# Kernel optimization log

Hardware: AMD Instinct MI355X
Metric: run time of the kernel (lower is better)

Reference implementation:

```python
import jax, jax.numpy as jnp
import numpy as np

C_IN, C_OUT = 64, 32
SD, RFF = 2, 16
RF = 0.05          # receptive_field percentile
TEMP = 1.0
EPS = 1e-8
RFF_STD = 6.0


def setup_inputs() -> dict:
    key = jax.random.key(0)
    ks = jax.random.split(key, 10)
    B_, T, V, Q = 2, 4, 2048, 512
    x = jax.random.normal(ks[0], (B_, T, V, C_IN), dtype=jnp.float32)
    pos = jax.random.uniform(ks[1], (V, SD), dtype=jnp.float32)
    query_pos = jax.random.uniform(ks[2], (Q, SD), dtype=jnp.float32)
    s = 1.0 / np.sqrt(C_IN)
    W_lin = jax.random.uniform(ks[3], (C_IN, C_IN), minval=-s, maxval=s, dtype=jnp.float32)
    b_lin = jax.random.uniform(ks[4], (C_IN,), minval=-s, maxval=s, dtype=jnp.float32)
    Bmat = RFF_STD * jax.random.normal(ks[5], (SD, RFF), dtype=jnp.float32)
    s1 = 1.0 / np.sqrt(32)
    W1 = jax.random.uniform(ks[6], (32, 32), minval=-s1, maxval=s1, dtype=jnp.float32)
    b1 = jax.random.uniform(ks[7], (32,), minval=-s1, maxval=s1, dtype=jnp.float32)
    W2 = jax.random.uniform(ks[8], (C_IN * C_OUT, 32), minval=-s1, maxval=s1, dtype=jnp.float32)
    sf = np.sqrt(3.0 / C_IN)
    filt = jax.random.uniform(ks[9], (C_IN * C_OUT,), minval=-sf, maxval=sf, dtype=jnp.float32)
    bias = jnp.zeros((C_OUT,), dtype=jnp.float32)
    return {"x": x, "pos": pos, "query_pos": query_pos, "W_lin": W_lin, "b_lin": b_lin,
            "Bmat": Bmat, "W1": W1, "b1": b1, "W2": W2, "filt": filt, "bias": bias}


def reference(x, pos, query_pos, W_lin, b_lin, Bmat, W1, b1, W2, filt, bias):
    # pairwise periodic displacement / squared distance
    dist = query_pos[:, None, :] - pos[None, :, :]            # (Q, V, 2)
    dist = (dist + 0.5) % 1.0 - 0.5                           # periodic wrap
    edist = jnp.sum(dist ** 2, axis=-1)                       # (Q, V)
    # quantile threshold -> max neighbourhood size (eager, data-dependent like torch)
    thr = jnp.quantile(edist, RF, axis=-1, keepdims=True)     # linear interpolation, as torch
    K = int(jnp.max(jnp.sum(edist <= thr, axis=-1)))
    _, ind = jax.lax.top_k(-edist, K)                         # (Q, K) nearest neighbours
    # gather per-query neighbour displacements / distances
    d_g = jnp.take_along_axis(dist, ind[..., None], axis=1)   # (Q, K, 2)
    e_g = jnp.take_along_axis(edist, ind, axis=1)[..., None]  # (Q, K, 1)
    e_g = e_g - jnp.min(e_g, axis=-2, keepdims=True)
    e_g = e_g / (jnp.max(e_g, axis=-2, keepdims=True) + EPS)
    k_dist = jax.nn.softmax(-e_g / TEMP, axis=-2)             # (Q, K, 1)
    # random Fourier features + kernel MLP
    proj = 2.0 * jnp.pi * (d_g @ Bmat)                        # (Q, K, 16)
    kfeat = jnp.concatenate([jnp.sin(proj), jnp.cos(proj)], axis=-1)  # (Q, K, 32)
    h = jax.nn.gelu(kfeat @ W1.T + b1, approximate=False)
    ker = (h @ W2.T + filt) * k_dist                          # (Q, K, C_IN*C_OUT)
    ker = ker.reshape(ker.shape[0], ker.shape[1], C_IN, C_OUT)
    # point-wise linear on features, then gather + contract
    xl = x @ W_lin.T + b_lin                                  # (B, T, V, C_IN)
    xg = xl[:, :, ind, :]                                     # (B, T, Q, K, C_IN)
    return jnp.einsum('qvcd,btqvc->btqd', ker, xg) + bias     # (B, T, Q, C_OUT)
```

## Files before the change

### kernel.cpp

```cpp
#include <hip/hip_runtime.h>

#define K_SEL 103
typedef unsigned long long ull_t;
typedef _Float16 f16x8 __attribute__((ext_vector_type(8)));
typedef float f32x4 __attribute__((ext_vector_type(4)));

__global__ __launch_bounds__(256, 4) void k12(const float* __restrict__ pos,
                                              const float* __restrict__ qpos,
                                              const float* __restrict__ Bmat,
                                              const float* __restrict__ W1,
                                              const float* __restrict__ b1,
                                              _Float16* __restrict__ Hh,
                                              int* __restrict__ indg,
                                              float* __restrict__ invtot,
                                              const float* __restrict__ x,
                                              const float* __restrict__ W,
                                              const float* __restrict__ b,
                                              _Float16* __restrict__ xlh,
                                              const float* __restrict__ W2,
                                              const float* __restrict__ filt,
                                              _Float16* __restrict__ W2th) {
    __shared__ __align__(16) unsigned char smem[30848];
    const int tid = threadIdx.x;
    const int bid = blockIdx.x;
    const int lane = tid & 63;
    const int wid = tid >> 6;

    if (bid >= 512) {
        const int bb = bid - 512;
        float* Wt = (float*)smem;
        if (tid < 132) {
            int t = bb * 132 + tid;
            int d = t & 31;
            int e = t >> 5;
            int c = e & 63;
            int j = e >> 6;
            float v = (j < 32) ? W2[(c * 32 + d) * 32 + j] : filt[c * 32 + d];
            W2th[d * 2112 + e] = (_Float16)v;
        }
        for (int t = tid; t < 4096; t += 256)
            Wt[(t & 63) * 65 + (t >> 6)] = W[t];
        __syncthreads();
        const int i = tid & 63;
        const int sub = tid >> 6;
        const float bi = b[i];
        #pragma unroll
        for (int rr = 0; rr < 2; ++rr) {
            const int r0 = bb * 32 + rr * 16 + sub * 4;
            float acc0 = bi, acc1 = bi, acc2 = bi, acc3 = bi;
            const float* xr = x + (size_t)r0 * 64;
            #pragma unroll 4
            for (int jj = 0; jj < 16; ++jj) {
                float4 v0 = *(const float4*)(xr + 0 * 64 + jj * 4);
                float4 v1 = *(const float4*)(xr + 1 * 64 + jj * 4);
                float4 v2 = *(const float4*)(xr + 2 * 64 + jj * 4);
                float4 v3 = *(const float4*)(xr + 3 * 64 + jj * 4);
                float w0 = Wt[(jj * 4 + 0) * 65 + i];
                float w1 = Wt[(jj * 4 + 1) * 65 + i];
                float w2 = Wt[(jj * 4 + 2) * 65 + i];
                float w3 = Wt[(jj * 4 + 3) * 65 + i];
                acc0 += v0.x * w0 + v0.y * w1 + v0.z * w2 + v0.w * w3;
                acc1 += v1.x * w0 + v1.y * w1 + v1.z * w2 + v1.w * w3;
                acc2 += v2.x * w0 + v2.y * w1 + v2.z * w2 + v2.w * w3;
                acc3 += v3.x * w0 + v3.y * w1 + v3.z * w2 + v3.w * w3;
            }
            xlh[(size_t)(r0 + 0) * 64 + i] = (_Float16)acc0;
            xlh[(size_t)(r0 + 1) * 64 + i] = (_Float16)acc1;
            xlh[(size_t)(r0 + 2) * 64 + i] = (_Float16)acc2;
            xlh[(size_t)(r0 + 3) * 64 + i] = (_Float16)acc3;
        }
        return;
    }

    const int q = bid;
    unsigned* ebits   = (unsigned*)(smem);
    unsigned* hist    = (unsigned*)(smem + 8192);
    _Float16* Hs      = (_Float16*)(smem + 8192);
    float*    W1s     = (float*)(smem + 24576);
    float*    b1s     = (float*)(smem + 28672);
    float*    Bm      = (float*)(smem + 28800);
    int*      sel_v   = (int*)(smem + 28928);
    float*    sel_e   = (float*)(smem + 29344);
    ull_t*    bnd     = (ull_t*)(smem + 29760);
    int*      counters= (int*)(smem + 30784);
    int*      info    = (int*)(smem + 30792);
    float*    wred    = (float*)(smem + 30800);
    float*    emax_s  = (float*)(smem + 30816);
    unsigned* wscan   = (unsigned*)(smem + 30824);

    for (int t = tid; t < 1024; t += 256) W1s[t] = W1[t];
    if (tid < 32) { b1s[tid] = b1[tid]; Bm[tid] = Bmat[tid]; }
    if (tid < 2)  counters[tid] = 0;
    for (int t = tid; t < 1024; t += 256) ((uint4*)hist)[t] = make_uint4(0, 0, 0, 0);
    const float qp0 = qpos[q * 2 + 0];
    const float qp1 = qpos[q * 2 + 1];
    __syncthreads();

    float lmin = 1e30f;
    for (int v = tid; v < 2048; v += 256) {
        float2 p = ((const float2*)pos)[v];
        float d0 = qp0 - p.x;
        float d1 = qp1 - p.y;
        d0 += 0.5f; d0 -= floorf(d0); d0 -= 0.5f;
        d1 += 0.5f; d1 -= floorf(d1); d1 -= 0.5f;
        float e = d0 * d0 + d1 * d1;
        ebits[v] = __float_as_uint(e);
        lmin = fminf(lmin, e);
        int bb2 = (int)(e * 8192.0f); bb2 = (bb2 > 4095) ? 4095 : bb2;
        atomicAdd(&hist[bb2], 1u);
    }
    #pragma unroll
    for (int off = 32; off > 0; off >>= 1)
        lmin = fminf(lmin, __shfl_xor(lmin, off, 64));
    if (lane == 0) wred[wid] = lmin;
    __syncthreads();
    const float e_min = fminf(fminf(wred[0], wred[1]), fminf(wred[2], wred[3]));

    unsigned lsum = 0;
    #pragma unroll
    for (int i = 0; i < 16; ++i) lsum += hist[tid * 16 + i];
    unsigned vq = lsum;
    #pragma unroll
    for (int off = 1; off < 64; off <<= 1) {
        unsigned n = __shfl_up(vq, off, 64);
        if (lane >= off) vq += n;
    }
    if (lane == 63) wscan[wid] = vq;
    __syncthreads();
    unsigned base = 0;
    for (int w2 = 0; w2 < wid; ++w2) base += wscan[w2];
    unsigned cum = base + vq - lsum;
    #pragma unroll
    for (int i = 0; i < 16; ++i) {
        unsigned cnt = hist[tid * 16 + i];
        if (cum <= 102u && 102u < cum + cnt) { info[0] = tid * 16 + i; info[1] = (int)cum; }
        cum += cnt;
    }
    __syncthreads();
    const int Bstar = info[0];
    const int L = info[1];
    const int need = K_SEL - L;

    {
        f16x8 z = {0, 0, 0, 0, 0, 0, 0, 0};
        for (int t = tid; t < 768; t += 256) ((f16x8*)Hs)[t] = z;
    }
    for (int v = tid; v < 2048; v += 256) {
        unsigned bb2 = ebits[v];
        float e = __uint_as_float(bb2);
        int bin = (int)(e * 8192.0f); bin = (bin > 4095) ? 4095 : bin;
        if (bin < Bstar) {
            int s2 = atomicAdd(&counters[0], 1);
            sel_v[s2] = v; sel_e[s2] = e;
        } else if (bin == Bstar) {
            int s2 = atomicAdd(&counters[1], 1);
            if (s2 < 128) bnd[s2] = (((ull_t)bb2) << 32) | (unsigned)v;
        }
    }
    __syncthreads();
    if (tid == 0) {
        int nb = counters[1]; if (nb > 128) nb = 128;
        for (int i = 1; i < nb; ++i) {
            ull_t key = bnd[i]; int j2 = i - 1;
            while (j2 >= 0 && bnd[j2] > key) { bnd[j2 + 1] = bnd[j2]; --j2; }
            bnd[j2 + 1] = key;
        }
        for (int i = 0; i < need; ++i) {
            sel_v[L + i] = (int)(unsigned)(bnd[i] & 0xffffffffull);
            sel_e[L + i] = __uint_as_float((unsigned)(bnd[i] >> 32));
        }
        emax_s[0] = __uint_as_float((unsigned)(bnd[need - 1] >> 32));
    }
    __syncthreads();

    const float denom = (emax_s[0] - e_min) + 1e-8f;
    float w = 0.0f;
    if (tid < K_SEL) {
        w = __expf(-(sel_e[tid] - e_min) / denom);
        sel_e[tid] = w;
    }
    float sw = w;
    #pragma unroll
    for (int off = 32; off > 0; off >>= 1)
        sw += __shfl_xor(sw, off, 64);
    if (lane == 0) wred[wid] = sw;
    __syncthreads();
    if (tid == 0)
        invtot[q] = 1.0f / (wred[0] + wred[1] + wred[2] + wred[3]);

    if (tid < 2 * K_SEL) {
        const int k = tid >> 1;
        const int io = (tid & 1) * 16;
        const int v = sel_v[k];
        const float wk = sel_e[k];
        float2 p = ((const float2*)pos)[v];
        float d0 = qp0 - p.x;
        float d1 = qp1 - p.y;
        d0 += 0.5f; d0 -= floorf(d0); d0 -= 0.5f;
        d1 += 0.5f; d1 -= floorf(d1); d1 -= 0.5f;
        float kf[32];
        #pragma unroll
        for (int f = 0; f < 16; ++f) {
            float t = d0 * Bm[f] + d1 * Bm[16 + f];
            float r = t - rintf(t);
            kf[f]      = __builtin_amdgcn_sinf(r);
            kf[16 + f] = __builtin_amdgcn_cosf(r);
        }
        #pragma unroll 4
        for (int i = io; i < io + 16; ++i) {
            float pre = b1s[i];
            #pragma unroll
            for (int jf = 0; jf < 32; ++jf) pre += kf[jf] * W1s[i * 32 + jf];
            float g = 0.5f * pre * (1.0f + erff(pre * 0.70710678118654752f));
            Hs[i * 128 + k] = (_Float16)(g * wk);
        }
        if (io == 0) {
            Hs[32 * 128 + k] = (_Float16)wk;
            indg[q * K_SEL + k] = v;
        }
    }
    __syncthreads();
    {
        _Float16* hq = Hh + (size_t)q * 6144;
        for (int t = tid; t < 768; t += 256)
            ((f16x8*)hq)[t] = ((const f16x8*)Hs)[t];
    }
}

__global__ __launch_bounds__(256, 4) void k3_main(const _Float16* __restrict__ xlh,
                                                  const _Float16* __restrict__ Hh,
                                                  const int* __restrict__ indg,
                                                  const _Float16* __restrict__ W2th,
                                                  const float* __restrict__ bias,
                                                  const float* __restrict__ invtot,
                                                  float* __restrict__ out) {
    const int bid = blockIdx.x;
    const int q = bid >> 1;
    const int bt0 = (bid & 1) * 4;
    const int tid = threadIdx.x;
    const int lane = tid & 63;
    const int wv = tid >> 6;
    const int n0 = lane & 15;
    const int quad = lane >> 4;

    __shared__ __align__(16) unsigned char smem[34944];
    _Float16* Xg  = (_Float16*)smem;
    _Float16* Zh4 = (_Float16*)(smem + 17536);
    int* ind_s    = (int*)(smem + 34432);
    float* red    = (float*)smem;

    const _Float16* hq = Hh + (size_t)q * 6144;
    f16x8 afr[4][3];
    #pragma unroll
    for (int ks = 0; ks < 4; ++ks)
        #pragma unroll
        for (int r = 0; r < 3; ++r)
            afr[ks][r] = *(const f16x8*)(hq + (r * 16 + n0) * 128 + ks * 32 + quad * 8);
    const float it = invtot[q];
    const int e0f = wv * 32 + quad * 8;
    f16x8 pf0 = *(const f16x8*)(W2th + (size_t)(0 * 16 + n0) * 2112 + e0f);
    f16x8 pf1 = *(const f16x8*)(W2th + (size_t)(1 * 16 + n0) * 2112 + e0f);
    if (tid < 128) {
        int kk = (tid < K_SEL) ? tid : tid - K_SEL;
        ind_s[tid] = indg[q * K_SEL + kk];
    }
    __syncthreads();

    int g_k[4], g_oct[4];
    #pragma unroll
    for (int i = 0; i < 4; ++i) {
        int t = tid + i * 256;
        g_k[i] = t >> 3;
        g_oct[i] = t & 7;
    }

    {
        f16x8 v0[4];
        #pragma unroll
        for (int i = 0; i < 4; ++i)
            v0[i] = *(const f16x8*)(xlh + ((size_t)bt0 * 2048 + ind_s[g_k[i]]) * 64 + g_oct[i] * 8);
        #pragma unroll
        for (int i = 0; i < 4; ++i) {
            int base = g_oct[i] * 1096 + g_k[i];
            #pragma unroll
            for (int jj = 0; jj < 8; ++jj) Xg[base + 136 * jj] = v0[i][jj];
        }
    }
    __syncthreads();

    const int cA = wv * 16 + n0;
    const int cswz = cA * 136 + ((cA >> 3) << 3);

    #pragma unroll
    for (int p = 0; p < 4; ++p) {
        f16x8 vn[4];
        if (p < 3) {
            #pragma unroll
            for (int i = 0; i < 4; ++i)
                vn[i] = *(const f16x8*)(xlh + ((size_t)(bt0 + p + 1) * 2048 + ind_s[g_k[i]]) * 64 + g_oct[i] * 8);
        }
        f32x4 Dz[3];
        #pragma unroll
        for (int r = 0; r < 3; ++r) Dz[r] = (f32x4){0.f, 0.f, 0.f, 0.f};
        #pragma unroll
        for (int ks = 0; ks < 4; ++ks) {
            f16x8 bfr = *(const f16x8*)(&Xg[cswz + ks * 32 + quad * 8]);
            #pragma unroll
            for (int r = 0; r < 3; ++r)
                Dz[r] = __builtin_amdgcn_mfma_f32_16x16x32_f16(afr[ks][r], bfr, Dz[r], 0, 0, 0);
        }
        __syncthreads();
        #pragma unroll
        for (int r = 0; r < 3; ++r)
            #pragma unroll
            for (int reg = 0; reg < 4; ++reg) {
                int j = r * 16 + quad * 4 + reg;
                if (j < 33) Zh4[p * 2112 + j * 64 + cA] = (_Float16)Dz[r][reg];
            }
        if (p < 3) {
            #pragma unroll
            for (int i = 0; i < 4; ++i) {
                int base = g_oct[i] * 1096 + g_k[i];
                #pragma unroll
                for (int jj = 0; jj < 8; ++jj) Xg[base + 136 * jj] = vn[i][jj];
            }
            __syncthreads();
        }
    }
    __syncthreads();

    f32x4 D2[2][2];
    #pragma unroll
    for (int pp = 0; pp < 2; ++pp)
        #pragma unroll
        for (int dt = 0; dt < 2; ++dt) D2[pp][dt] = (f32x4){0.f, 0.f, 0.f, 0.f};
    {
        f16x8 a2 = {0, 0, 0, 0, 0, 0, 0, 0};
        if (n0 < 4) a2 = *(const f16x8*)(&Zh4[n0 * 2112 + e0f]);
        D2[0][0] = __builtin_amdgcn_mfma_f32_16x16x32_f16(a2, pf0, D2[0][0], 0, 0, 0);
        D2[0][1] = __builtin_amdgcn_mfma_f32_16x16x32_f16(a2, pf1, D2[0][1], 0, 0, 0);
    }
    int pp = 1;
    #pragma unroll 2
    for (int s = wv + 4; s < 66; s += 4) {
        const int e0 = s * 32 + quad * 8;
        f16x8 a2 = {0, 0, 0, 0, 0, 0, 0, 0};
        if (n0 < 4) a2 = *(const f16x8*)(&Zh4[n0 * 2112 + e0]);
        #pragma unroll
        for (int dt = 0; dt < 2; ++dt) {
            f16x8 bfr = *(const f16x8*)(W2th + (size_t)(dt * 16 + n0) * 2112 + e0);
            D2[pp][dt] = __builtin_amdgcn_mfma_f32_16x16x32_f16(a2, bfr, D2[pp][dt], 0, 0, 0);
        }
        pp ^= 1;
    }
    #pragma unroll
    for (int dt = 0; dt < 2; ++dt)
        D2[0][dt] = D2[0][dt] + D2[1][dt];

    if (quad == 0) {
        #pragma unroll
        for (int dt = 0; dt < 2; ++dt)
            #pragma unroll
            for (int reg = 0; reg < 4; ++reg)
                red[((wv * 2 + dt) * 4 + reg) * 16 + n0] = D2[0][dt][reg];
    }
    __syncthreads();
    if (tid < 128) {
        const int bt = tid >> 5;
        const int d = tid & 31;
        const int dt = d >> 4;
        const int dn = d & 15;
        float s = 0.0f;
        #pragma unroll
        for (int w2 = 0; w2 < 4; ++w2)
            s += red[((w2 * 2 + dt) * 4 + bt) * 16 + dn];
        out[((size_t)(bt0 + bt) * 512 + q) * 32 + d] = bias[d] + it * s;
    }
}

extern "C" void kernel_launch(void* const* d_in, const int* in_sizes, int n_in,
                              void* d_out, int out_size, void* d_ws, size_t ws_size,
                              hipStream_t stream) {
    const float* x     = (const float*)d_in[0];
    const float* pos   = (const float*)d_in[1];
    const float* qpos  = (const float*)d_in[2];
    const float* W_lin = (const float*)d_in[3];
    const float* b_lin = (const float*)d_in[4];
    const float* Bmat  = (const float*)d_in[5];
    const float* W1    = (const float*)d_in[6];
    const float* b1    = (const float*)d_in[7];
    const float* W2    = (const float*)d_in[8];
    const float* filt  = (const float*)d_in[9];
    const float* bias  = (const float*)d_in[10];
    float* out = (float*)d_out;

    float* ws = (float*)d_ws;
    _Float16* xlh    = (_Float16*)ws;
    _Float16* Hh     = (_Float16*)(ws + 524288);
    int*      indg   = (int*)(ws + 2097152);
    _Float16* W2th   = (_Float16*)(ws + 2150144);
    float*    invtot = ws + 2183936;

    k12<<<1024, 256, 0, stream>>>(pos, qpos, Bmat, W1, b1, Hh, indg, invtot,
                                  x, W_lin, b_lin, xlh, W2, filt, W2th);
    k3_main<<<1024, 256, 0, stream>>>(xlh, Hh, indg, W2th, bias, invtot, out);
}
```

Baseline: 121.2 us.

## Fuse the two kernels into one launch synchronized by global flags

Merges the neighbour-selection/MLP kernel and the contraction kernel into a single kernel. After its first-phase work, each block signals completion with release atomics: a per-query flag for the query blocks, a shared counter for the linear-projection blocks. It then spin-waits on its query's flag and on all 512 projection blocks before running the contraction phase. This removes the kernel boundary and lets work overlap, but it adds a memset launch, spin-wait latency, and a reliance on all 1024 blocks being co-resident to avoid deadlock.

```diff
diff --git a/kernel.cpp b/kernel.cpp
--- a/kernel.cpp
+++ b/kernel.cpp
@@ -5,22 +5,19 @@
 typedef _Float16 f16x8 __attribute__((ext_vector_type(8)));
 typedef float f32x4 __attribute__((ext_vector_type(4)));
 
-__global__ __launch_bounds__(256, 4) void k12(const float* __restrict__ pos,
-                                              const float* __restrict__ qpos,
-                                              const float* __restrict__ Bmat,
-                                              const float* __restrict__ W1,
-                                              const float* __restrict__ b1,
-                                              _Float16* __restrict__ Hh,
-                                              int* __restrict__ indg,
-                                              float* __restrict__ invtot,
-                                              const float* __restrict__ x,
-                                              const float* __restrict__ W,
-                                              const float* __restrict__ b,
-                                              _Float16* __restrict__ xlh,
-                                              const float* __restrict__ W2,
-                                              const float* __restrict__ filt,
-                                              _Float16* __restrict__ W2th) {
-    __shared__ __align__(16) unsigned char smem[30848];
+__global__ __launch_bounds__(256, 4) void fused(
+    const float* __restrict__ pos, const float* __restrict__ qpos,
+    const float* __restrict__ Bmat, const float* __restrict__ W1,
+    const float* __restrict__ b1, const float* __restrict__ x,
+    const float* __restrict__ W, const float* __restrict__ b,
+    const float* __restrict__ W2, const float* __restrict__ filt,
+    const float* __restrict__ bias,
+    _Float16* __restrict__ xlh, _Float16* __restrict__ Hh,
+    int* __restrict__ indg, float* __restrict__ invtot,
+    _Float16* __restrict__ W2th, int* __restrict__ flags,
+    int* __restrict__ k1ctr, float* __restrict__ out)
+{
+    __shared__ __align__(16) unsigned char smem[34944];
     const int tid = threadIdx.x;
     const int bid = blockIdx.x;
     const int lane = tid & 63;
@@ -69,200 +66,204 @@
             xlh[(size_t)(r0 + 2) * 64 + i] = (_Float16)acc2;
             xlh[(size_t)(r0 + 3) * 64 + i] = (_Float16)acc3;
         }
-        return;
-    }
-
-    const int q = bid;
-    unsigned* ebits   = (unsigned*)(smem);
-    unsigned* hist    = (unsigned*)(smem + 8192);
-    _Float16* Hs      = (_Float16*)(smem + 8192);
-    float*    W1s     = (float*)(smem + 24576);
-    float*    b1s     = (float*)(smem + 28672);
-    float*    Bm      = (float*)(smem + 28800);
-    int*      sel_v   = (int*)(smem + 28928);
-    float*    sel_e   = (float*)(smem + 29344);
-    ull_t*    bnd     = (ull_t*)(smem + 29760);
-    int*      counters= (int*)(smem + 30784);
-    int*      info    = (int*)(smem + 30792);
-    float*    wred    = (float*)(smem + 30800);
-    float*    emax_s  = (float*)(smem + 30816);
-    unsigned* wscan   = (unsigned*)(smem + 30824);
-
-    for (int t = tid; t < 1024; t += 256) W1s[t] = W1[t];
-    if (tid < 32) { b1s[tid] = b1[tid]; Bm[tid] = Bmat[tid]; }
-    if (tid < 2)  counters[tid] = 0;
-    for (int t = tid; t < 1024; t += 256) ((uint4*)hist)[t] = make_uint4(0, 0, 0, 0);
-    const float qp0 = qpos[q * 2 + 0];
-    const float qp1 = qpos[q * 2 + 1];
-    __syncthreads();
-
-    float lmin = 1e30f;
-    for (int v = tid; v < 2048; v += 256) {
-        float2 p = ((const float2*)pos)[v];
-        float d0 = qp0 - p.x;
-        float d1 = qp1 - p.y;
-        d0 += 0.5f; d0 -= floorf(d0); d0 -= 0.5f;
-        d1 += 0.5f; d1 -= floorf(d1); d1 -= 0.5f;
-        float e = d0 * d0 + d1 * d1;
-        ebits[v] = __float_as_uint(e);
-        lmin = fminf(lmin, e);
-        int bb2 = (int)(e * 8192.0f); bb2 = (bb2 > 4095) ? 4095 : bb2;
-        atomicAdd(&hist[bb2], 1u);
-    }
-    #pragma unroll
-    for (int off = 32; off > 0; off >>= 1)
-        lmin = fminf(lmin, __shfl_xor(lmin, off, 64));
-    if (lane == 0) wred[wid] = lmin;
-    __syncthreads();
-    const float e_min = fminf(fminf(wred[0], wred[1]), fminf(wred[2], wred[3]));
-
-    unsigned lsum = 0;
-    #pragma unroll
-    for (int i = 0; i < 16; ++i) lsum += hist[tid * 16 + i];
-    unsigned vq = lsum;
-    #pragma unroll
-    for (int off = 1; off < 64; off <<= 1) {
-        unsigned n = __shfl_up(vq, off, 64);
-        if (lane >= off) vq += n;
-    }
-    if (lane == 63) wscan[wid] = vq;
-    __syncthreads();
-    unsigned base = 0;
-    for (int w2 = 0; w2 < wid; ++w2) base += wscan[w2];
-    unsigned cum = base + vq - lsum;
-    #pragma unroll
-    for (int i = 0; i < 16; ++i) {
-        unsigned cnt = hist[tid * 16 + i];
-        if (cum <= 102u && 102u < cum + cnt) { info[0] = tid * 16 + i; info[1] = (int)cum; }
-        cum += cnt;
-    }
-    __syncthreads();
-    const int Bstar = info[0];
-    const int L = info[1];
-    const int need = K_SEL - L;
-
-    {
-        f16x8 z = {0, 0, 0, 0, 0, 0, 0, 0};
-        for (int t = tid; t < 768; t += 256) ((f16x8*)Hs)[t] = z;
-    }
-    for (int v = tid; v < 2048; v += 256) {
-        unsigned bb2 = ebits[v];
-        float e = __uint_as_float(bb2);
-        int bin = (int)(e * 8192.0f); bin = (bin > 4095) ? 4095 : bin;
-        if (bin < Bstar) {
-            int s2 = atomicAdd(&counters[0], 1);
-            sel_v[s2] = v; sel_e[s2] = e;
-        } else if (bin == Bstar) {
-            int s2 = atomicAdd(&counters[1], 1);
-            if (s2 < 128) bnd[s2] = (((ull_t)bb2) << 32) | (unsigned)v;
-        }
-    }
+    } else {
+        const int q = bid;
+        unsigned* ebits   = (unsigned*)(smem);
+        unsigned* hist    = (unsigned*)(smem + 8192);
+        _Float16* Hs      = (_Float16*)(smem + 8192);
+        float*    W1s     = (float*)(smem + 24576);
+        float*    b1s     = (float*)(smem + 28672);
+        float*    Bm      = (float*)(smem + 28800);
+        int*      sel_v   = (int*)(smem + 28928);
+        float*    sel_e   = (float*)(smem + 29344);
+        ull_t*    bnd     = (ull_t*)(smem + 29760);
+        int*      counters= (int*)(smem + 30784);
+        int*      info    = (int*)(smem + 30792);
+        float*    wred    = (float*)(smem + 30800);
+        float*    emax_s  = (float*)(smem + 30816);
+        unsigned* wscan   = (unsigned*)(smem + 30824);
+
+        for (int t = tid; t < 1024; t += 256) W1s[t] = W1[t];
+        if (tid < 32) { b1s[tid] = b1[tid]; Bm[tid] = Bmat[tid]; }
+        if (tid < 2)  counters[tid] = 0;
+        for (int t = tid; t < 1024; t += 256) ((uint4*)hist)[t] = make_uint4(0, 0, 0, 0);
+        const float qp0 = qpos[q * 2 + 0];
+        const float qp1 = qpos[q * 2 + 1];
+        __syncthreads();
+
+        float lmin = 1e30f;
+        for (int v = tid; v < 2048; v += 256) {
+            float2 p = ((const float2*)pos)[v];
+            float d0 = qp0 - p.x;
+            float d1 = qp1 - p.y;
+            d0 += 0.5f; d0 -= floorf(d0); d0 -= 0.5f;
+            d1 += 0.5f; d1 -= floorf(d1); d1 -= 0.5f;
+            float e = d0 * d0 + d1 * d1;
+            ebits[v] = __float_as_uint(e);
+            lmin = fminf(lmin, e);
+            int bb2 = (int)(e * 8192.0f); bb2 = (bb2 > 4095) ? 4095 : bb2;
+            atomicAdd(&hist[bb2], 1u);
+        }
+        #pragma unroll
+        for (int off = 32; off > 0; off >>= 1)
+            lmin = fminf(lmin, __shfl_xor(lmin, off, 64));
+        if (lane == 0) wred[wid] = lmin;
+        __syncthreads();
+        const float e_min = fminf(fminf(wred[0], wred[1]), fminf(wred[2], wred[3]));
+
+        unsigned lsum = 0;
+        #pragma unroll
+        for (int i = 0; i < 16; ++i) lsum += hist[tid * 16 + i];
+        unsigned vq = lsum;
+        #pragma unroll
+        for (int off = 1; off < 64; off <<= 1) {
+            unsigned n = __shfl_up(vq, off, 64);
+            if (lane >= off) vq += n;
+        }
+        if (lane == 63) wscan[wid] = vq;
+        __syncthreads();
+        unsigned base = 0;
+        for (int w2 = 0; w2 < wid; ++w2) base += wscan[w2];
+        unsigned cum = base + vq - lsum;
+        #pragma unroll
+        for (int i = 0; i < 16; ++i) {
+            unsigned cnt = hist[tid * 16 + i];
+            if (cum <= 102u && 102u < cum + cnt) { info[0] = tid * 16 + i; info[1] = (int)cum; }
+            cum += cnt;
+        }
+        __syncthreads();
+        const int Bstar = info[0];
+        const int L = info[1];
+        const int need = K_SEL - L;
+
+        {
+            f16x8 z = {0, 0, 0, 0, 0, 0, 0, 0};
+            for (int t = tid; t < 768; t += 256) ((f16x8*)Hs)[t] = z;
+        }
+        for (int v = tid; v < 2048; v += 256) {
+            unsigned bb2 = ebits[v];
+            float e = __uint_as_float(bb2);
+            int bin = (int)(e * 8192.0f); bin = (bin > 4095) ? 4095 : bin;
+            if (bin < Bstar) {
+                int s2 = atomicAdd(&counters[0], 1);
+                sel_v[s2] = v; sel_e[s2] = e;
+            } else if (bin == Bstar) {
+                int s2 = atomicAdd(&counters[1], 1);
+                if (s2 < 128) bnd[s2] = (((ull_t)bb2) << 32) | (unsigned)v;
+            }
+        }
+        __syncthreads();
+        if (tid == 0) {
+            int nb = counters[1]; if (nb > 128) nb = 128;
+            for (int i = 1; i < nb; ++i) {
+                ull_t key = bnd[i]; int j2 = i - 1;
+                while (j2 >= 0 && bnd[j2] > key) { bnd[j2 + 1] = bnd[j2]; --j2; }
+                bnd[j2 + 1] = key;
+            }
+            for (int i = 0; i < need; ++i) {
+                sel_v[L + i] = (int)(unsigned)(bnd[i] & 0xffffffffull);
+                sel_e[L + i] = __uint_as_float((unsigned)(bnd[i] >> 32));
+            }
+            emax_s[0] = __uint_as_float((unsigned)(bnd[need - 1] >> 32));
+        }
+        __syncthreads();
+
+        const float denom = (emax_s[0] - e_min) + 1e-8f;
+        float w = 0.0f;
+        if (tid < K_SEL) {
+            w = __expf(-(sel_e[tid] - e_min) / denom);
+            sel_e[tid] = w;
+        }
+        float sw = w;
+        #pragma unroll
+        for (int off = 32; off > 0; off >>= 1)
+            sw += __shfl_xor(sw, off, 64);
+        if (lane == 0) wred[wid] = sw;
+        __syncthreads();
+        if (tid == 0)
+            invtot[q] = 1.0f / (wred[0] + wred[1] + wred[2] + wred[3]);
+
+        if (tid < 2 * K_SEL) {
+            const int k = tid >> 1;
+            const int io = (tid & 1) * 16;
+            const int v = sel_v[k];
+            const float wk = sel_e[k];
+            float2 p = ((const float2*)pos)[v];
+            float d0 = qp0 - p.x;
+            float d1 = qp1 - p.y;
+            d0 += 0.5f; d0 -= floorf(d0); d0 -= 0.5f;
+            d1 += 0.5f; d1 -= floorf(d1); d1 -= 0.5f;
+            float kf[32];
+            #pragma unroll
+            for (int f = 0; f < 16; ++f) {
+                float t = d0 * Bm[f] + d1 * Bm[16 + f];
+                float r = t - rintf(t);
+                kf[f]      = __builtin_amdgcn_sinf(r);
+                kf[16 + f] = __builtin_amdgcn_cosf(r);
+            }
+            #pragma unroll 4
+            for (int i = io; i < io + 16; ++i) {
+                float pre = b1s[i];
+                #pragma unroll
+                for (int jf = 0; jf < 32; ++jf) pre += kf[jf] * W1s[i * 32 + jf];
+                float g = 0.5f * pre * (1.0f + erff(pre * 0.70710678118654752f));
+                Hs[i * 128 + k] = (_Float16)(g * wk);
+            }
+            if (io == 0) {
+                Hs[32 * 128 + k] = (_Float16)wk;
+                indg[q * K_SEL + k] = v;
+            }
+        }
+        __syncthreads();
+        {
+            _Float16* hq = Hh + (size_t)q * 6144;
+            for (int t = tid; t < 768; t += 256)
+                ((f16x8*)hq)[t] = ((const f16x8*)Hs)[t];
+        }
+    }
+
+    __threadfence();
     __syncthreads();
     if (tid == 0) {
-        int nb = counters[1]; if (nb > 128) nb = 128;
-        for (int i = 1; i < nb; ++i) {
-            ull_t key = bnd[i]; int j2 = i - 1;
-            while (j2 >= 0 && bnd[j2] > key) { bnd[j2 + 1] = bnd[j2]; --j2; }
-            bnd[j2 + 1] = key;
-        }
-        for (int i = 0; i < need; ++i) {
-            sel_v[L + i] = (int)(unsigned)(bnd[i] & 0xffffffffull);
-            sel_e[L + i] = __uint_as_float((unsigned)(bnd[i] >> 32));
-        }
-        emax_s[0] = __uint_as_float((unsigned)(bnd[need - 1] >> 32));
-    }
-    __syncthreads();
-
-    const float denom = (emax_s[0] - e_min) + 1e-8f;
-    float w = 0.0f;
-    if (tid < K_SEL) {
-        w = __expf(-(sel_e[tid] - e_min) / denom);
-        sel_e[tid] = w;
-    }
-    float sw = w;
-    #pragma unroll
-    for (int off = 32; off > 0; off >>= 1)
-        sw += __shfl_xor(sw, off, 64);
-    if (lane == 0) wred[wid] = sw;
-    __syncthreads();
-    if (tid == 0)
-        invtot[q] = 1.0f / (wred[0] + wred[1] + wred[2] + wred[3]);
-
-    if (tid < 2 * K_SEL) {
-        const int k = tid >> 1;
-        const int io = (tid & 1) * 16;
-        const int v = sel_v[k];
-        const float wk = sel_e[k];
-        float2 p = ((const float2*)pos)[v];
-        float d0 = qp0 - p.x;
-        float d1 = qp1 - p.y;
-        d0 += 0.5f; d0 -= floorf(d0); d0 -= 0.5f;
-        d1 += 0.5f; d1 -= floorf(d1); d1 -= 0.5f;
-        float kf[32];
-        #pragma unroll
-        for (int f = 0; f < 16; ++f) {
-            float t = d0 * Bm[f] + d1 * Bm[16 + f];
-            float r = t - rintf(t);
-            kf[f]      = __builtin_amdgcn_sinf(r);
-            kf[16 + f] = __builtin_amdgcn_cosf(r);
-        }
-        #pragma unroll 4
-        for (int i = io; i < io + 16; ++i) {
-            float pre = b1s[i];
-            #pragma unroll
-            for (int jf = 0; jf < 32; ++jf) pre += kf[jf] * W1s[i * 32 + jf];
-            float g = 0.5f * pre * (1.0f + erff(pre * 0.70710678118654752f));
-            Hs[i * 128 + k] = (_Float16)(g * wk);
-        }
-        if (io == 0) {
-            Hs[32 * 128 + k] = (_Float16)wk;
-            indg[q * K_SEL + k] = v;
-        }
-    }
-    __syncthreads();
-    {
-        _Float16* hq = Hh + (size_t)q * 6144;
-        for (int t = tid; t < 768; t += 256)
-            ((f16x8*)hq)[t] = ((const f16x8*)Hs)[t];
-    }
-}
-
-__global__ __launch_bounds__(256, 4) void k3_main(const _Float16* __restrict__ xlh,
-                                                  const _Float16* __restrict__ Hh,
-                                                  const int* __restrict__ indg,
-                                                  const _Float16* __restrict__ W2th,
-                                                  const float* __restrict__ bias,
-                                                  const float* __restrict__ invtot,
-                                                  float* __restrict__ out) {
-    const int bid = blockIdx.x;
-    const int q = bid >> 1;
+        if (bid < 512)
+            __hip_atomic_store(&flags[bid], 1, __ATOMIC_RELEASE, __HIP_MEMORY_SCOPE_AGENT);
+        else
+            __hip_atomic_fetch_add(k1ctr, 1, __ATOMIC_ACQ_REL, __HIP_MEMORY_SCOPE_AGENT);
+    }
+    const int q2 = bid >> 1;
+    if (tid == 0) {
+        while (__hip_atomic_load(&flags[q2], __ATOMIC_ACQUIRE, __HIP_MEMORY_SCOPE_AGENT) == 0)
+            __builtin_amdgcn_s_sleep(2);
+        while (__hip_atomic_load(k1ctr, __ATOMIC_ACQUIRE, __HIP_MEMORY_SCOPE_AGENT) < 512)
+            __builtin_amdgcn_s_sleep(2);
+    }
+    __syncthreads();
+    __threadfence();
+
     const int bt0 = (bid & 1) * 4;
-    const int tid = threadIdx.x;
-    const int lane = tid & 63;
-    const int wv = tid >> 6;
     const int n0 = lane & 15;
     const int quad = lane >> 4;
-
-    __shared__ __align__(16) unsigned char smem[34944];
+    const int wv = wid;
+
     _Float16* Xg  = (_Float16*)smem;
     _Float16* Zh4 = (_Float16*)(smem + 17536);
     int* ind_s    = (int*)(smem + 34432);
     float* red    = (float*)smem;
 
-    const _Float16* hq = Hh + (size_t)q * 6144;
+    const _Float16* hq = Hh + (size_t)q2 * 6144;
     f16x8 afr[4][3];
     #pragma unroll
     for (int ks = 0; ks < 4; ++ks)
         #pragma unroll
         for (int r = 0; r < 3; ++r)
             afr[ks][r] = *(const f16x8*)(hq + (r * 16 + n0) * 128 + ks * 32 + quad * 8);
-    const float it = invtot[q];
+    const float it = invtot[q2];
     const int e0f = wv * 32 + quad * 8;
     f16x8 pf0 = *(const f16x8*)(W2th + (size_t)(0 * 16 + n0) * 2112 + e0f);
     f16x8 pf1 = *(const f16x8*)(W2th + (size_t)(1 * 16 + n0) * 2112 + e0f);
     if (tid < 128) {
         int kk = (tid < K_SEL) ? tid : tid - K_SEL;
-        ind_s[tid] = indg[q * K_SEL + kk];
+        ind_s[tid] = indg[q2 * K_SEL + kk];
     }
     __syncthreads();
 
@@ -374,7 +375,7 @@
         #pragma unroll
         for (int w2 = 0; w2 < 4; ++w2)
             s += red[((w2 * 2 + dt) * 4 + bt) * 16 + dn];
-        out[((size_t)(bt0 + bt) * 512 + q) * 32 + d] = bias[d] + it * s;
+        out[((size_t)(bt0 + bt) * 512 + q2) * 32 + d] = bias[d] + it * s;
     }
 }
 
@@ -400,8 +401,13 @@
     int*      indg   = (int*)(ws + 2097152);
     _Float16* W2th   = (_Float16*)(ws + 2150144);
     float*    invtot = ws + 2183936;
-
-    k12<<<1024, 256, 0, stream>>>(pos, qpos, Bmat, W1, b1, Hh, indg, invtot,
-                                  x, W_lin, b_lin, xlh, W2, filt, W2th);
-    k3_main<<<1024, 256, 0, stream>>>(xlh, Hh, indg, W2th, bias, invtot, out);
+    int*      flags  = (int*)(ws + 2184448);
+    int*      k1ctr  = (int*)(ws + 2184960);
+
+    hipMemsetAsync((void*)flags, 0, 513 * sizeof(int), stream);
+
+    void* nothing = nullptr; (void)nothing;
+    fused<<<1024, 256, 0, stream>>>(pos, qpos, Bmat, W1, b1, x, W_lin, b_lin,
+                                    W2, filt, bias, xlh, Hh, indg, invtot,
+                                    W2th, flags, k1ctr, out);
 }
```

Measured after the change: 326.3 us. 169% more time.
